# Performance work log

Hardware: AMD Instinct MI355X
Metric: run time of the kernel (lower is better)

The kernel has to match this reference:

```python
import jax, jax.numpy as jnp
import numpy as np

N = 262144  # number of candidate occluded-object feature rows

def _w(k, shape, fan_in):
    return jax.random.normal(k, shape, jnp.float32) * (1.0 / np.sqrt(fan_in))

def setup_inputs() -> dict:
    key = jax.random.key(0)
    ks = jax.random.split(key, 5)
    return {
        "select_feature": jax.random.normal(ks[0], (N, 512), jnp.float32),
        # Conv2d(512,256,1x1) == Linear(512->256); Conv2d(256,128,1x1) == Linear(256->128)
        "W1": _w(ks[1], (256, 512), 512), "b1": jnp.zeros((256,), jnp.float32),
        "W2": _w(ks[2], (128, 256), 256), "b2": jnp.zeros((128,), jnp.float32),
        "Wf1": _w(ks[3], (64, 128), 128), "bf1": jnp.zeros((64,), jnp.float32),
        "Wf2": _w(ks[4], (2, 64), 64),   "bf2": jnp.zeros((2,), jnp.float32),
    }

def reference(select_feature, W1, b1, W2, b2, Wf1, bf1, Wf2, bf2):
    # masker_train: unsqueeze->1x1 convs->squeeze is exactly a per-row MLP.
    h = jax.nn.relu(select_feature @ W1.T + b1)   # [N,256]
    h = jax.nn.relu(h @ W2.T + b2)                # [N,128]
    h = jax.nn.relu(h @ Wf1.T + bf1)              # [N,64]
    logits = h @ Wf2.T + bf2                      # [N,2]
    return jax.nn.softmax(logits, axis=-1)
```

## Files before the change

### kernel.cpp

```cpp
#include <hip/hip_runtime.h>
#include <hip/hip_bf16.h>

typedef __bf16 bf16x8 __attribute__((ext_vector_type(8)));
typedef float  f32x4  __attribute__((ext_vector_type(4)));

#define MFMA16(a, b, c) __builtin_amdgcn_mfma_f32_16x16x32_bf16((a), (b), (c), 0, 0, 0)

__device__ __forceinline__ f32x4 nt_load4(const float* p) {
    return __builtin_nontemporal_load((const f32x4*)p);
}

__global__ void prep_weights(const float* __restrict__ W1, const float* __restrict__ W2,
                             const float* __restrict__ Wf1, const float* __restrict__ Wf2,
                             __bf16* __restrict__ w1p, __bf16* __restrict__ w2p,
                             __bf16* __restrict__ wf1p, __bf16* __restrict__ wf2b) {
    int t = blockIdx.x * 256 + threadIdx.x;
    int lane = t & 63, m16 = lane & 15, q = (lane >> 4) & 3;
    if (t < 16384) {
        int ct = (t >> 6) & 15, ks = t >> 10;
        const float* s = W1 + (size_t)(ct * 16 + m16) * 512 + ks * 32 + q * 8;
        __bf16* d = w1p + (size_t)t * 8;
        for (int j = 0; j < 8; ++j) d[j] = (__bf16)s[j];
    }
    if (t < 4096) {
        int ct = (t >> 6) & 7, ks = t >> 9;
        const float* s = W2 + (size_t)(ct * 16 + m16) * 256 + ks * 32 + q * 8;
        __bf16* d = w2p + (size_t)t * 8;
        for (int j = 0; j < 8; ++j) d[j] = (__bf16)s[j];
    }
    if (t < 1024) {
        int ct = (t >> 6) & 3, ks = t >> 8;
        const float* s = Wf1 + (size_t)(ct * 16 + m16) * 128 + ks * 32 + q * 8;
        __bf16* d = wf1p + (size_t)t * 8;
        for (int j = 0; j < 8; ++j) d[j] = (__bf16)s[j];
    }
    if (t < 128) wf2b[t] = (__bf16)Wf2[t];
}

__global__ __launch_bounds__(256, 2)
void mlp_kernel(const float* __restrict__ X,
                const __bf16* __restrict__ w1p,  const float* __restrict__ b1,
                const __bf16* __restrict__ w2p,  const float* __restrict__ b2,
                const __bf16* __restrict__ wf1p, const float* __restrict__ bf1,
                const __bf16* __restrict__ wf2b, const float* __restrict__ bf2,
                float* __restrict__ out) {
    __shared__ __align__(16) __bf16 hbuf[4][32][264];

    const int lane = threadIdx.x & 63;
    const int wave = threadIdx.x >> 6;
    const int m16  = lane & 15;
    const int q    = lane >> 4;
    const int row0 = blockIdx.x * 128 + wave * 32;
    __bf16(*hw)[264] = hbuf[wave];

    f32x4 C1[2][16];
#pragma unroll
    for (int rt = 0; rt < 2; ++rt)
#pragma unroll
        for (int ct = 0; ct < 16; ++ct) C1[rt][ct] = (f32x4){0.f, 0.f, 0.f, 0.f};

    const float* xr0 = X + (size_t)(row0 + m16) * 512 + q * 8;
    const float* xr1 = xr0 + (size_t)16 * 512;
    f32x4 x00 = nt_load4(xr0);
    f32x4 x01 = nt_load4(xr0 + 4);
    f32x4 x10 = nt_load4(xr1);
    f32x4 x11 = nt_load4(xr1 + 4);

#pragma unroll
    for (int ks = 0; ks < 16; ++ks) {
        __builtin_amdgcn_s_barrier();
        const __bf16* wp = w1p + (size_t)ks * 8192 + lane * 8;
        bf16x8 b0[8], b1v[8];
#pragma unroll
        for (int ct = 0; ct < 8; ++ct)
            b0[ct] = *(const bf16x8*)(wp + ct * 512);

        bf16x8 a0, a1;
        a0[0] = (__bf16)x00[0]; a0[1] = (__bf16)x00[1]; a0[2] = (__bf16)x00[2]; a0[3] = (__bf16)x00[3];
        a0[4] = (__bf16)x01[0]; a0[5] = (__bf16)x01[1]; a0[6] = (__bf16)x01[2]; a0[7] = (__bf16)x01[3];
        a1[0] = (__bf16)x10[0]; a1[1] = (__bf16)x10[1]; a1[2] = (__bf16)x10[2]; a1[3] = (__bf16)x10[3];
        a1[4] = (__bf16)x11[0]; a1[5] = (__bf16)x11[1]; a1[6] = (__bf16)x11[2]; a1[7] = (__bf16)x11[3];

        if (ks < 15) {
            x00 = nt_load4(xr0 + (ks + 1) * 32);
            x01 = nt_load4(xr0 + (ks + 1) * 32 + 4);
            x10 = nt_load4(xr1 + (ks + 1) * 32);
            x11 = nt_load4(xr1 + (ks + 1) * 32 + 4);
        }
#pragma unroll
        for (int ct = 0; ct < 8; ++ct)
            b1v[ct] = *(const bf16x8*)(wp + (8 + ct) * 512);

#pragma unroll
        for (int ct = 0; ct < 8; ++ct) {
            C1[0][ct] = MFMA16(a0, b0[ct], C1[0][ct]);
            C1[1][ct] = MFMA16(a1, b0[ct], C1[1][ct]);
        }
#pragma unroll
        for (int ct = 0; ct < 8; ++ct) {
            C1[0][8 + ct] = MFMA16(a0, b1v[ct], C1[0][8 + ct]);
            C1[1][8 + ct] = MFMA16(a1, b1v[ct], C1[1][8 + ct]);
        }
    }
#pragma unroll
    for (int ct = 0; ct < 16; ++ct) {
        float bias = b1[ct * 16 + m16];
#pragma unroll
        for (int rt = 0; rt < 2; ++rt)
#pragma unroll
            for (int r = 0; r < 4; ++r) {
                float v = C1[rt][ct][r] + bias;
                v = v > 0.f ? v : 0.f;
                hw[rt * 16 + q * 4 + r][ct * 16 + m16] = (__bf16)v;
            }
    }

    f32x4 C2[2][8];
#pragma unroll
    for (int rt = 0; rt < 2; ++rt)
#pragma unroll
        for (int ct = 0; ct < 8; ++ct) C2[rt][ct] = (f32x4){0.f, 0.f, 0.f, 0.f};

#pragma unroll
    for (int ks = 0; ks < 8; ++ks) {
        __builtin_amdgcn_s_barrier();
        const __bf16* wp = w2p + (size_t)ks * 4096 + lane * 8;
        bf16x8 b[8];
#pragma unroll
        for (int ct = 0; ct < 8; ++ct) b[ct] = *(const bf16x8*)(wp + ct * 512);
        bf16x8 a0 = *(const bf16x8*)&hw[m16][ks * 32 + q * 8];
        bf16x8 a1 = *(const bf16x8*)&hw[16 + m16][ks * 32 + q * 8];
#pragma unroll
        for (int ct = 0; ct < 8; ++ct) {
            C2[0][ct] = MFMA16(a0, b[ct], C2[0][ct]);
            C2[1][ct] = MFMA16(a1, b[ct], C2[1][ct]);
        }
    }
#pragma unroll
    for (int ct = 0; ct < 8; ++ct) {
        float bias = b2[ct * 16 + m16];
#pragma unroll
        for (int rt = 0; rt < 2; ++rt)
#pragma unroll
            for (int r = 0; r < 4; ++r) {
                float v = C2[rt][ct][r] + bias;
                v = v > 0.f ? v : 0.f;
                hw[rt * 16 + q * 4 + r][ct * 16 + m16] = (__bf16)v;
            }
    }

    f32x4 C3[2][4];
#pragma unroll
    for (int rt = 0; rt < 2; ++rt)
#pragma unroll
        for (int ct = 0; ct < 4; ++ct) C3[rt][ct] = (f32x4){0.f, 0.f, 0.f, 0.f};

#pragma unroll
    for (int ks = 0; ks < 4; ++ks) {
        __builtin_amdgcn_s_barrier();
        const __bf16* wp = wf1p + (size_t)ks * 2048 + lane * 8;
        bf16x8 b[4];
#pragma unroll
        for (int ct = 0; ct < 4; ++ct) b[ct] = *(const bf16x8*)(wp + ct * 512);
        bf16x8 a0 = *(const bf16x8*)&hw[m16][ks * 32 + q * 8];
        bf16x8 a1 = *(const bf16x8*)&hw[16 + m16][ks * 32 + q * 8];
#pragma unroll
        for (int ct = 0; ct < 4; ++ct) {
            C3[0][ct] = MFMA16(a0, b[ct], C3[0][ct]);
            C3[1][ct] = MFMA16(a1, b[ct], C3[1][ct]);
        }
    }
#pragma unroll
    for (int ct = 0; ct < 4; ++ct) {
        float bias = bf1[ct * 16 + m16];
#pragma unroll
        for (int rt = 0; rt < 2; ++rt)
#pragma unroll
            for (int r = 0; r < 4; ++r) {
                float v = C3[rt][ct][r] + bias;
                v = v > 0.f ? v : 0.f;
                hw[rt * 16 + q * 4 + r][ct * 16 + m16] = (__bf16)v;
            }
    }

    {
        const int r = lane >> 1;
        const int c = lane & 1;
        float dot = 0.f;
#pragma unroll
        for (int j8 = 0; j8 < 8; ++j8) {
            bf16x8 hv = *(const bf16x8*)&hw[r][j8 * 8];
            bf16x8 wv = *(const bf16x8*)(wf2b + c * 64 + j8 * 8);
#pragma unroll
            for (int j = 0; j < 8; ++j) dot += (float)hv[j] * (float)wv[j];
        }
        float logit = dot + bf2[c];
        float other = __shfl_xor(logit, 1, 64);
        float mx = fmaxf(logit, other);
        float e0 = expf(logit - mx);
        float e1 = expf(other - mx);
        __builtin_nontemporal_store(e0 / (e0 + e1), &out[(size_t)(row0 + r) * 2 + c]);
    }
}

extern "C" void kernel_launch(void* const* d_in, const int* in_sizes, int n_in,
                              void* d_out, int out_size, void* d_ws, size_t ws_size,
                              hipStream_t stream) {
    const float* X   = (const float*)d_in[0];
    const float* W1  = (const float*)d_in[1];
    const float* b1  = (const float*)d_in[2];
    const float* W2  = (const float*)d_in[3];
    const float* b2  = (const float*)d_in[4];
    const float* Wf1 = (const float*)d_in[5];
    const float* bf1 = (const float*)d_in[6];
    const float* Wf2 = (const float*)d_in[7];
    const float* bf2 = (const float*)d_in[8];
    float* out = (float*)d_out;

    const int N = in_sizes[0] / 512;

    __bf16* w1p  = (__bf16*)d_ws;
    __bf16* w2p  = w1p  + 131072;
    __bf16* wf1p = w2p  + 32768;
    __bf16* wf2b = wf1p + 8192;

    prep_weights<<<64, 256, 0, stream>>>(W1, W2, Wf1, Wf2, w1p, w2p, wf1p, wf2b);
    mlp_kernel<<<N / 128, 256, 0, stream>>>(X, w1p, b1, w2p, b2, wf1p, bf1,
                                            wf2b, bf2, out);
}
```

Measured before the change: 794.1 us.

## Stage weights into LDS via async global_load_lds double-buffering, 512-thread blocks

Weight tiles for all three MFMA layers are now copied cooperatively into double-buffered shared memory with global_load_lds, prefetching the next k-slice while the current one is consumed. Previously each wave loaded weights straight from global/L2. Blocks grow to 8 waves and 256 rows so each staged weight slice is shared by more waves. This adds explicit vmcnt waits and a barrier per k-step, and uses about 150KB of LDS per block, which may limit occupancy to one block per CU.

```diff
diff --git a/kernel.cpp b/kernel.cpp
--- a/kernel.cpp
+++ b/kernel.cpp
@@ -5,6 +5,12 @@
 typedef float  f32x4  __attribute__((ext_vector_type(4)));
 
 #define MFMA16(a, b, c) __builtin_amdgcn_mfma_f32_16x16x32_bf16((a), (b), (c), 0, 0, 0)
+
+#define GLDS16(gp, lp) __builtin_amdgcn_global_load_lds(                      \
+    (const __attribute__((address_space(1))) void*)(gp),                      \
+    (__attribute__((address_space(3))) void*)(lp), 16, 0, 0)
+#define SBAR()   __builtin_amdgcn_s_barrier()
+#define SCHED0() __builtin_amdgcn_sched_barrier(0)
 
 __device__ __forceinline__ f32x4 nt_load4(const float* p) {
     return __builtin_nontemporal_load((const f32x4*)p);
@@ -37,21 +43,21 @@
     if (t < 128) wf2b[t] = (__bf16)Wf2[t];
 }
 
-__global__ __launch_bounds__(256, 2)
+__global__ __launch_bounds__(512, 2)
 void mlp_kernel(const float* __restrict__ X,
                 const __bf16* __restrict__ w1p,  const float* __restrict__ b1,
                 const __bf16* __restrict__ w2p,  const float* __restrict__ b2,
                 const __bf16* __restrict__ wf1p, const float* __restrict__ bf1,
                 const __bf16* __restrict__ wf2b, const float* __restrict__ bf2,
                 float* __restrict__ out) {
-    __shared__ __align__(16) __bf16 hbuf[4][32][264];
+    __shared__ __align__(16) __bf16 smem[75776];
 
     const int lane = threadIdx.x & 63;
     const int wave = threadIdx.x >> 6;
     const int m16  = lane & 15;
     const int q    = lane >> 4;
-    const int row0 = blockIdx.x * 128 + wave * 32;
-    __bf16(*hw)[264] = hbuf[wave];
+    const int row0 = blockIdx.x * 256 + wave * 32;
+    __bf16(*hw)[264] = (__bf16(*)[264])&smem[wave * 8448];
 
     f32x4 C1[2][16];
 #pragma unroll
@@ -61,19 +67,39 @@
 
     const float* xr0 = X + (size_t)(row0 + m16) * 512 + q * 8;
     const float* xr1 = xr0 + (size_t)16 * 512;
+
+    {
+        const char* g = (const char*)w1p + wave * 2048 + lane * 16;
+        GLDS16(g,        &smem[wave * 1024]);
+        GLDS16(g + 1024, &smem[wave * 1024 + 512]);
+    }
+    SCHED0();
     f32x4 x00 = nt_load4(xr0);
     f32x4 x01 = nt_load4(xr0 + 4);
     f32x4 x10 = nt_load4(xr1);
     f32x4 x11 = nt_load4(xr1 + 4);
+    asm volatile("s_waitcnt vmcnt(4)" ::: "memory");
+    SBAR(); SCHED0();
 
 #pragma unroll
     for (int ks = 0; ks < 16; ++ks) {
-        __builtin_amdgcn_s_barrier();
-        const __bf16* wp = w1p + (size_t)ks * 8192 + lane * 8;
+        const __bf16* wl = &smem[(ks & 1) * 8192 + lane * 8];
+        if (ks < 15) {
+            const char* g = (const char*)w1p + (size_t)(ks + 1) * 16384
+                          + wave * 2048 + lane * 16;
+            __bf16* l = &smem[((ks + 1) & 1) * 8192 + wave * 1024];
+            GLDS16(g, l);
+            GLDS16(g + 1024, l + 512);
+        } else {
+            const char* g = (const char*)w2p + wave * 1024 + lane * 16;
+            GLDS16(g, &smem[67584 + wave * 512]);
+        }
+        SCHED0();
+
         bf16x8 b0[8], b1v[8];
 #pragma unroll
         for (int ct = 0; ct < 8; ++ct)
-            b0[ct] = *(const bf16x8*)(wp + ct * 512);
+            b0[ct] = *(const bf16x8*)(wl + ct * 512);
 
         bf16x8 a0, a1;
         a0[0] = (__bf16)x00[0]; a0[1] = (__bf16)x00[1]; a0[2] = (__bf16)x00[2]; a0[3] = (__bf16)x00[3];
@@ -89,7 +115,7 @@
         }
 #pragma unroll
         for (int ct = 0; ct < 8; ++ct)
-            b1v[ct] = *(const bf16x8*)(wp + (8 + ct) * 512);
+            b1v[ct] = *(const bf16x8*)(wl + (8 + ct) * 512);
 
 #pragma unroll
         for (int ct = 0; ct < 8; ++ct) {
@@ -101,6 +127,13 @@
             C1[0][8 + ct] = MFMA16(a0, b1v[ct], C1[0][8 + ct]);
             C1[1][8 + ct] = MFMA16(a1, b1v[ct], C1[1][8 + ct]);
         }
+
+        if (ks < 15) {
+            asm volatile("s_waitcnt vmcnt(4)" ::: "memory");
+        } else {
+            asm volatile("s_waitcnt vmcnt(0)" ::: "memory");
+        }
+        SBAR(); SCHED0();
     }
 #pragma unroll
     for (int ct = 0; ct < 16; ++ct) {
@@ -123,11 +156,20 @@
 
 #pragma unroll
     for (int ks = 0; ks < 8; ++ks) {
-        __builtin_amdgcn_s_barrier();
-        const __bf16* wp = w2p + (size_t)ks * 4096 + lane * 8;
+        const __bf16* wl = &smem[67584 + (ks & 1) * 4096 + lane * 8];
+        if (ks < 7) {
+            const char* g = (const char*)w2p + (size_t)(ks + 1) * 8192
+                          + wave * 1024 + lane * 16;
+            GLDS16(g, &smem[67584 + ((ks + 1) & 1) * 4096 + wave * 512]);
+        } else {
+            const char* g = (const char*)wf1p + wave * 1024 + lane * 16;
+            GLDS16(g, &smem[67584 + wave * 512]);
+        }
+        SCHED0();
         bf16x8 b[8];
 #pragma unroll
-        for (int ct = 0; ct < 8; ++ct) b[ct] = *(const bf16x8*)(wp + ct * 512);
+        for (int ct = 0; ct < 8; ++ct)
+            b[ct] = *(const bf16x8*)(wl + ct * 512);
         bf16x8 a0 = *(const bf16x8*)&hw[m16][ks * 32 + q * 8];
         bf16x8 a1 = *(const bf16x8*)&hw[16 + m16][ks * 32 + q * 8];
 #pragma unroll
@@ -135,6 +177,12 @@
             C2[0][ct] = MFMA16(a0, b[ct], C2[0][ct]);
             C2[1][ct] = MFMA16(a1, b[ct], C2[1][ct]);
         }
+        asm volatile("s_waitcnt vmcnt(0)" ::: "memory");
+        SBAR(); SCHED0();
+    }
+    {
+        const char* g = (const char*)wf1p + 8192 + wave * 1024 + lane * 16;
+        GLDS16(g, &smem[71680 + wave * 512]);
     }
 #pragma unroll
     for (int ct = 0; ct < 8; ++ct) {
@@ -157,11 +205,15 @@
 
 #pragma unroll
     for (int ks = 0; ks < 4; ++ks) {
-        __builtin_amdgcn_s_barrier();
-        const __bf16* wp = wf1p + (size_t)ks * 2048 + lane * 8;
+        if (ks == 2) {
+            asm volatile("s_waitcnt vmcnt(0)" ::: "memory");
+            SBAR(); SCHED0();
+        }
+        const __bf16* wl = &smem[67584 + ks * 2048 + lane * 8];
         bf16x8 b[4];
 #pragma unroll
-        for (int ct = 0; ct < 4; ++ct) b[ct] = *(const bf16x8*)(wp + ct * 512);
+        for (int ct = 0; ct < 4; ++ct)
+            b[ct] = *(const bf16x8*)(wl + ct * 512);
         bf16x8 a0 = *(const bf16x8*)&hw[m16][ks * 32 + q * 8];
         bf16x8 a1 = *(const bf16x8*)&hw[16 + m16][ks * 32 + q * 8];
 #pragma unroll
@@ -225,6 +277,6 @@
     __bf16* wf2b = wf1p + 8192;
 
     prep_weights<<<64, 256, 0, stream>>>(W1, W2, Wf1, Wf2, w1p, w2p, wf1p, wf2b);
-    mlp_kernel<<<N / 128, 256, 0, stream>>>(X, w1p, b1, w2p, b2, wf1p, bf1,
+    mlp_kernel<<<N / 256, 512, 0, stream>>>(X, w1p, b1, w2p, b2, wf1p, bf1,
                                             wf2b, bf2, out);
 }
```

Measured after the change: 752.5 us. 1.06x faster.
